# Optimization experiments

Hardware: AMD Instinct MI355X
Metric: run time of the kernel (lower is better)

The kernel has to match this reference:

```python
import jax, jax.numpy as jnp
import numpy as np

WS, OWS, NH = 16, 24, 2          # window size, overlap window size (=int(16*0.5)+16), num heads
PAD = (OWS - WS) // 2            # unfold padding = 4


def conv2d(x, w, b):
    kh, kw = w.shape[2], w.shape[3]
    out = jax.lax.conv_general_dilated(x, w, (1, 1), [(kh // 2, kh // 2), (kw // 2, kw // 2)],
                                       dimension_numbers=('NCHW', 'OIHW', 'NCHW'))
    return out + b[None, :, None, None]


def layer_norm(x, g, b, eps=1e-5):
    m = x.mean(-1, keepdims=True)
    v = ((x - m) ** 2).mean(-1, keepdims=True)
    return (x - m) * jax.lax.rsqrt(v + eps) * g + b


def stem(depth, cw1, cb1, cw2, cb2, cw3, cb3, cw4, cb4, in_g, in_b):
    # BasicConv(1->8,k3,relu) -> (8->16,k1,relu) -> (16->16,k3,relu) -> (16->32,k1) -> InstanceNorm2d(32,affine)
    y = jax.nn.relu(conv2d(depth, cw1, cb1))
    y = jax.nn.relu(conv2d(y, cw2, cb2))
    y = jax.nn.relu(conv2d(y, cw3, cb3))
    y = conv2d(y, cw4, cb4)
    m = y.mean((2, 3), keepdims=True)
    v = ((y - m) ** 2).mean((2, 3), keepdims=True)
    return (y - m) * jax.lax.rsqrt(v + 1e-5) * in_g[None, :, None, None] + in_b[None, :, None, None]


def ocab(xq, ykv, rpi, n1g, n1b, wq, bq, wkv, bkv, rpb, wp, bp, n2g, n2b, mw1, mb1, mw2, mb2):
    # Overlapping cross-attention block (HAT-style OCAB, cross variant: q from xq, kv from ykv).
    b, c, h, w = xq.shape
    x = xq.transpose(0, 2, 3, 1)   # b h w c
    y = ykv.transpose(0, 2, 3, 1)
    shortcut = x
    q = layer_norm(x, n1g, n1b) @ wq + bq          # b h w c
    kv = layer_norm(y, n1g, n1b) @ wkv + bkv       # b h w 2c
    nhw, nww = h // WS, w // WS
    # non-overlapping query windows: (b*nw, WS*WS, c)
    qw = q.reshape(b, nhw, WS, nww, WS, c).transpose(0, 1, 3, 2, 4, 5).reshape(b * nhw * nww, WS * WS, c)
    # overlapping kv windows via unfold (patch channel order = (channel, kh, kw), same as torch unfold)
    patches = jax.lax.conv_general_dilated_patches(kv.transpose(0, 3, 1, 2), (OWS, OWS), (WS, WS),
                                                   [(PAD, PAD), (PAD, PAD)])  # b, 2c*OWS*OWS, nhw, nww
    patches = patches.reshape(b, 2, c, OWS * OWS, nhw * nww).transpose(1, 0, 4, 3, 2).reshape(2, b * nhw * nww, OWS * OWS, c)
    k, v = patches[0], patches[1]
    d = c // NH
    qh = qw.reshape(-1, WS * WS, NH, d).transpose(0, 2, 1, 3) * (d ** -0.5)
    kh = k.reshape(-1, OWS * OWS, NH, d).transpose(0, 2, 1, 3)
    vh = v.reshape(-1, OWS * OWS, NH, d).transpose(0, 2, 1, 3)
    attn = jnp.einsum('whqd,whkd->whqk', qh, kh)
    attn = attn + rpb[rpi].transpose(2, 0, 1)[None]  # rel-pos bias -> [1, NH, WS*WS, OWS*OWS]
    attn = jax.nn.softmax(attn, axis=-1)
    out = jnp.einsum('whqk,whkd->whqd', attn, vh).transpose(0, 2, 1, 3).reshape(-1, WS * WS, c)
    # window reverse
    out = out.reshape(b, nhw, nww, WS, WS, c).transpose(0, 1, 3, 2, 4, 5).reshape(b, h, w, c)
    out = out @ wp + bp + shortcut
    out = out + (jax.nn.gelu(layer_norm(out, n2g, n2b) @ mw1 + mb1) @ mw2 + mb2)  # mlp_ratio=2
    return out.transpose(0, 3, 1, 2)


def setup_inputs():
    key = jax.random.key(0)
    ks = jax.random.split(key, 16)
    B, C, H, W = 1, 32, 256, 256
    s = 0.05
    return dict(
        x=jax.random.normal(ks[0], (B, C, H, W), jnp.float32),
        depth=jax.random.normal(ks[1], (B, 1, H, W), jnp.float32),
        rpi=jax.random.randint(ks[2], (WS * WS, OWS * OWS), 0, (WS + OWS - 1) ** 2),
        cw1=jax.random.normal(ks[3], (8, 1, 3, 3)) * s, cb1=jnp.zeros(8),
        cw2=jax.random.normal(ks[4], (16, 8, 1, 1)) * s, cb2=jnp.zeros(16),
        cw3=jax.random.normal(ks[5], (16, 16, 3, 3)) * s, cb3=jnp.zeros(16),
        cw4=jax.random.normal(ks[6], (32, 16, 1, 1)) * s, cb4=jnp.zeros(32),
        in_g=jnp.ones(32), in_b=jnp.zeros(32),
        n1g=jnp.ones(C), n1b=jnp.zeros(C),
        wq=jax.random.normal(ks[7], (C, C)) * s, bq=jnp.zeros(C),
        wkv=jax.random.normal(ks[8], (C, 2 * C)) * s, bkv=jnp.zeros(2 * C),
        rpb=jax.random.normal(ks[9], ((WS + OWS - 1) ** 2, NH)) * 0.02,
        wp=jax.random.normal(ks[10], (C, C)) * s, bp=jnp.zeros(C),
        n2g=jnp.ones(C), n2b=jnp.zeros(C),
        mw1=jax.random.normal(ks[11], (C, 2 * C)) * s, mb1=jnp.zeros(2 * C),
        mw2=jax.random.normal(ks[12], (2 * C, C)) * s, mb2=jnp.zeros(C),
    )


def reference(x, depth, rpi, cw1, cb1, cw2, cb2, cw3, cb3, cw4, cb4, in_g, in_b,
              n1g, n1b, wq, bq, wkv, bkv, rpb, wp, bp, n2g, n2b, mw1, mb1, mw2, mb2):
    f = stem(depth, cw1, cb1, cw2, cb2, cw3, cb3, cw4, cb4, in_g, in_b)
    a = (n1g, n1b, wq, bq, wkv, bkv, rpb, wp, bp, n2g, n2b, mw1, mb1, mw2, mb2)
    out1 = ocab(x, f, rpi, *a)   # shared OCAB weights, called twice with swapped roles
    out2 = ocab(f, x, rpi, *a)
    return out1 + out2 + x
```

## Files before the change

### kernel.cpp

```cpp
#include <hip/hip_runtime.h>
#include <hip/hip_bf16.h>

#define HW 65536
#define KPAD 584

typedef __attribute__((ext_vector_type(8))) short bf8;
typedef __attribute__((ext_vector_type(4))) float f4;

__device__ __forceinline__ unsigned short f2b(float x) {
  unsigned int u = __float_as_uint(x);
  unsigned int r = (u + 0x7fff + ((u >> 16) & 1)) >> 16;
  return (unsigned short)r;
}
__device__ __forceinline__ unsigned int pk2(float lo, float hi) {
  return (__float_as_uint(hi) & 0xffff0000u) | (__float_as_uint(lo) >> 16);
}
__device__ __forceinline__ float ex2(float x) { return __builtin_amdgcn_exp2f(x); }

__device__ __forceinline__ void stem_front_body(
    int bx, int t, const float* __restrict__ depth,
    const float* __restrict__ cw1, const float* __restrict__ cb1,
    const float* __restrict__ cw2, const float* __restrict__ cb2,
    float* __restrict__ t2) {
  int p = bx * 256 + t;
  int y = p >> 8, x = p & 255;
  float in9[9];
#pragma unroll
  for (int ky = 0; ky < 3; ky++)
#pragma unroll
    for (int kx = 0; kx < 3; kx++) {
      int yy = y + ky - 1, xx = x + kx - 1;
      bool ok = ((unsigned)yy < 256u) && ((unsigned)xx < 256u);
      in9[ky*3+kx] = ok ? depth[yy*256+xx] : 0.f;
    }
  float t1[8];
#pragma unroll
  for (int o = 0; o < 8; o++) {
    float s = cb1[o];
#pragma unroll
    for (int i = 0; i < 9; i++) s += in9[i] * cw1[o*9+i];
    t1[o] = fmaxf(s, 0.f);
  }
#pragma unroll
  for (int o = 0; o < 16; o++) {
    float s = cb2[o];
#pragma unroll
    for (int ci = 0; ci < 8; ci++) s += t1[ci] * cw2[o*8+ci];
    t2[o*HW + p] = fmaxf(s, 0.f);
  }
}

__device__ __forceinline__ void bias_body(
    int bx, int t, const int* __restrict__ rpi,
    const float* __restrict__ rpb, float* __restrict__ biasT) {
  int idx = bx*256 + t;
  int hd = idx / 147456;
  int rem = idx - hd*147456;
  int qt = rem / 9216;
  int r2 = rem - qt*9216;
  int kb = r2 >> 6;
  int q16 = (r2 >> 2) & 15;
  int r = r2 & 3;
  int key = kb*4 + r;
  int qq = qt*16 + q16;
  biasT[idx] = (rpb[rpi[qq*576 + key]*2 + hd] - 8.0f) * 1.44269504f;
}

__device__ __forceinline__ void lnmm16_body(
    int role, int bx, int t,
    float* ws, float* gs, float* bs, float* b2s, float* as, float* bbs,
    const float* __restrict__ x, const float* __restrict__ t4,
    const float* __restrict__ part,
    const float* __restrict__ ig, const float* __restrict__ ib,
    const float* __restrict__ n1g, const float* __restrict__ n1b,
    const float* __restrict__ wq, const float* __restrict__ bq,
    const float* __restrict__ wkv, const float* __restrict__ bkv,
    float* q1, float* kv1, float* q2, float* kv2) {
  const float *src, *wm, *bo; float* dst;
  int wstride, wcol; bool ain;
  if (role < 6) { src = x;  ain = false; } else { src = t4; ain = true; }
  switch (role) {
    default:
    case 0:  wm=wq;  wstride=32; wcol=0;  bo=bq;  dst=q1;               break;
    case 1:  wm=wq;  wstride=32; wcol=16; bo=bq;  dst=q1+16*HW;         break;
    case 2: case 3: case 4: case 5:
             wm=wkv; wstride=64; wcol=16*(role-2); bo=bkv; dst=kv2+16*(role-2)*HW; break;
    case 6:  wm=wq;  wstride=32; wcol=0;  bo=bq;  dst=q2;               break;
    case 7:  wm=wq;  wstride=32; wcol=16; bo=bq;  dst=q2+16*HW;         break;
    case 8: case 9: case 10: case 11:
             wm=wkv; wstride=64; wcol=16*(role-8); bo=bkv; dst=kv1+16*(role-8)*HW; break;
  }
  for (int i = t; i < 512; i += 256) ws[i] = wm[(i>>4)*wstride + wcol + (i&15)];
  if (t < 16) b2s[t] = bo[wcol + t];
  if (t < 32) {
    gs[t] = n1g[t]; bs[t] = n1b[t];
    if (ain) {
      float s = 0.f, ss = 0.f;
#pragma unroll
      for (int k = 0; k < 16; k++) { s += part[t*16+k]; ss += part[512 + t*16+k]; }
      float m = s * (1.f/65536.f);
      float var = ss * (1.f/65536.f) - m*m;
      float a = rsqrtf(var + 1e-5f) * ig[t];
      as[t] = a; bbs[t] = ib[t] - m*a;
    }
  }
  __syncthreads();
  int p = bx*256 + t;
  float v[32]; float s = 0.f;
  if (ain) {
#pragma unroll
    for (int c = 0; c < 32; c++) { v[c] = src[c*HW+p]*as[c] + bbs[c]; s += v[c]; }
  } else {
#pragma unroll
    for (int c = 0; c < 32; c++) { v[c] = src[c*HW+p]; s += v[c]; }
  }
  float m = s * 0.03125f;
  float ss = 0.f;
#pragma unroll
  for (int c = 0; c < 32; c++) { float d = v[c]-m; ss += d*d; }
  float rs = rsqrtf(ss*0.03125f + 1e-5f);
  float acc[16];
#pragma unroll
  for (int j = 0; j < 16; j++) acc[j] = b2s[j];
#pragma unroll
  for (int c = 0; c < 32; c++) {
    float ln = (v[c]-m)*rs*gs[c] + bs[c];
    const float4* w4 = (const float4*)&ws[c*16];
#pragma unroll
    for (int j4 = 0; j4 < 4; j4++) {
      float4 w = w4[j4];
      acc[j4*4+0] += ln*w.x; acc[j4*4+1] += ln*w.y;
      acc[j4*4+2] += ln*w.z; acc[j4*4+3] += ln*w.w;
    }
  }
#pragma unroll
  for (int j = 0; j < 16; j++) dst[j*HW+p] = acc[j];
}

__global__ __launch_bounds__(256) void k_misc(
    const float* __restrict__ depth,
    const float* __restrict__ cw1, const float* __restrict__ cb1,
    const float* __restrict__ cw2, const float* __restrict__ cb2,
    float* __restrict__ t2,
    const int* __restrict__ rpi, const float* __restrict__ rpb, float* __restrict__ biasT,
    const float* __restrict__ x, const float* __restrict__ t4, const float* __restrict__ part,
    const float* __restrict__ ig, const float* __restrict__ ib,
    const float* __restrict__ n1g, const float* __restrict__ n1b,
    const float* __restrict__ wq, const float* __restrict__ bq,
    const float* __restrict__ wkv, const float* __restrict__ bkv,
    float* q1, float* kv1, float* q2, float* kv2) {
  __shared__ __align__(16) float ws[512];
  __shared__ float gs[32], bs[32], b2s[16], as[32], bbs[32];
  int id = blockIdx.x, t = threadIdx.x;
  if (id < 256) { stem_front_body(id, t, depth, cw1, cb1, cw2, cb2, t2); return; }
  if (id < 1408) { bias_body(id - 256, t, rpi, rpb, biasT); return; }
  int r = id - 1408;
  lnmm16_body(r >> 8, r & 255, t, ws, gs, bs, b2s, as, bbs,
              x, t4, part, ig, ib, n1g, n1b, wq, bq, wkv, bkv, q1, kv1, q2, kv2);
}

__global__ __launch_bounds__(256) void k_lnmmB(
    const float* __restrict__ x, const float* __restrict__ t4, const float* __restrict__ part,
    const float* __restrict__ ig, const float* __restrict__ ib,
    const float* __restrict__ n1g, const float* __restrict__ n1b,
    const float* __restrict__ wq, const float* __restrict__ bq,
    const float* __restrict__ wkv, const float* __restrict__ bkv,
    float* q1, float* kv1, float* q2, float* kv2, int ybase) {
  __shared__ __align__(16) float ws[512];
  __shared__ float gs[32], bs[32], b2s[16], as[32], bbs[32];
  lnmm16_body(ybase + blockIdx.y, blockIdx.x, threadIdx.x, ws, gs, bs, b2s, as, bbs,
              x, t4, part, ig, ib, n1g, n1b, wq, bq, wkv, bkv, q1, kv1, q2, kv2);
}

__global__ __launch_bounds__(256) void k_conv3(
    const float* __restrict__ t2, const float* __restrict__ cw3,
    const float* __restrict__ cb3, float* __restrict__ t3) {
  int t = threadIdx.x;
  int p = blockIdx.x*256 + t;
  int og = blockIdx.y;
  int y = p >> 8, x = p & 255;
  float acc[4];
#pragma unroll
  for (int o = 0; o < 4; o++) acc[o] = cb3[og*4+o];
#pragma unroll 1
  for (int tap = 0; tap < 9; tap++) {
    int ky = tap/3 - 1, kx = tap - (tap/3)*3 - 1;
    int yy = y+ky, xx = x+kx;
    bool ok = ((unsigned)yy < 256u) && ((unsigned)xx < 256u);
    int pp = yy*256+xx;
#pragma unroll
    for (int ci = 0; ci < 16; ci++) {
      float v = ok ? t2[ci*HW+pp] : 0.f;
#pragma unroll
      for (int o = 0; o < 4; o++)
        acc[o] += v * cw3[(og*4+o)*144 + ci*9 + tap];
    }
  }
#pragma unroll
  for (int o = 0; o < 4; o++) t3[(og*4+o)*HW+p] = fmaxf(acc[o], 0.f);
}

__global__ __launch_bounds__(256) void k_conv4(
    const float* __restrict__ t3, const float* __restrict__ cw4,
    const float* __restrict__ cb4, float* __restrict__ t4) {
  int t = threadIdx.x;
  int p = blockIdx.x*256 + t;
  int og = blockIdx.y;
  float v[16];
#pragma unroll
  for (int ci = 0; ci < 16; ci++) v[ci] = t3[ci*HW+p];
#pragma unroll
  for (int o = 0; o < 8; o++) {
    int oo = og*8 + o;
    float s = cb4[oo];
#pragma unroll
    for (int ci = 0; ci < 16; ci++) s += v[ci]*cw4[oo*16+ci];
    t4[oo*HW+p] = s;
  }
}

__global__ __launch_bounds__(256) void k_instats1(const float* __restrict__ t4,
                                                  float* __restrict__ part) {
  int c = blockIdx.x >> 4, seg = blockIdx.x & 15;
  const float4* src = (const float4*)(t4 + c*HW + seg*4096);
  float s = 0.f, ss = 0.f;
  for (int i = threadIdx.x; i < 1024; i += 256) {
    float4 v = src[i];
    s  += v.x + v.y + v.z + v.w;
    ss += v.x*v.x + v.y*v.y + v.z*v.z + v.w*v.w;
  }
#pragma unroll
  for (int off = 32; off > 0; off >>= 1) {
    s  += __shfl_down(s, off, 64);
    ss += __shfl_down(ss, off, 64);
  }
  __shared__ float sh[8];
  int wid = threadIdx.x >> 6;
  if ((threadIdx.x & 63) == 0) { sh[wid] = s; sh[4+wid] = ss; }
  __syncthreads();
  if (threadIdx.x == 0) {
    part[blockIdx.x]       = sh[0]+sh[1]+sh[2]+sh[3];
    part[512 + blockIdx.x] = sh[4]+sh[5]+sh[6]+sh[7];
  }
}

__global__ __launch_bounds__(256, 4) void k_attn(
    const float* __restrict__ qA, const float* __restrict__ kvA, float* __restrict__ aoA,
    const float* __restrict__ qB, const float* __restrict__ kvB, float* __restrict__ aoB,
    const float* __restrict__ biasT) {
  __shared__ __align__(16) unsigned short Ks[576*16];
  __shared__ __align__(16) unsigned short Vt[16*KPAD];

  const float* q  = blockIdx.y ? qB  : qA;
  const float* kv = blockIdx.y ? kvB : kvA;
  float* ao       = blockIdx.y ? aoB : aoA;

  int id = blockIdx.x;
  int lin = ((id & 7) << 6) | (id >> 3);
  int wi = lin >> 1, hd = lin & 1;
  int wy = wi >> 4, wx = wi & 15;
  int t = threadIdx.x;
  int by = wy*16 - 4, bx = wx*16 - 4;
  int kbase = hd*16*HW, vbase = (32 + hd*16)*HW;

  int wave = t >> 6, lane = t & 63;
  int quad = lane >> 4, l16 = lane & 15;
  const bf8 zero8 = {0,0,0,0,0,0,0,0};

  bf8 qf[4];
#pragma unroll
  for (int qi = 0; qi < 4; qi++) {
    int qt = wave*4 + qi;
    if (quad < 2) {
      int prow = (wy*16 + qt)*256 + wx*16 + l16;
      unsigned short qtmp[8];
#pragma unroll
      for (int j = 0; j < 8; j++)
        qtmp[j] = f2b(q[(hd*16 + quad*8 + j)*HW + prow] * 0.360673503f);
      qf[qi] = *(const bf8*)qtmp;
    } else {
      qf[qi] = zero8;
    }
  }

  for (int e = t; e < 576; e += 256) {
    int dy = e / 24, dx = e - dy*24;
    int yy = by + dy, xx = bx + dx;
    bool ok = ((unsigned)yy < 256u) && ((unsigned)xx < 256u);
    int pp = yy*256 + xx;
    int off = e & 31;
    int ppos = ((off & 12) << 1) + ((off >> 4) << 2) + (off & 3);
    int vcol = (e & ~31) + ppos;
    unsigned short tk[16];
#pragma unroll
    for (int i = 0; i < 16; i++) {
      float kvl = ok ? kv[kbase + i*HW + pp] : 0.f;
      float vvl = ok ? kv[vbase + i*HW + pp] : 0.f;
      tk[i] = f2b(kvl);
      Vt[i*KPAD + vcol] = f2b(vvl);
    }
    *(uint4*)&Ks[e*16]     = *(uint4*)&tk[0];
    *(uint4*)&Ks[e*16 + 8] = *(uint4*)&tk[8];
  }
  __syncthreads();

  f4 oacc[4];
  float lr[4];
  const float* bb[4];
#pragma unroll
  for (int qi = 0; qi < 4; qi++) {
    int qt = wave*4 + qi;
    oacc[qi] = (f4){0.f,0.f,0.f,0.f};
    lr[qi] = 0.f;
    bb[qi] = biasT + (hd*16 + qt)*9216 + quad*64 + l16*4;
  }

#pragma unroll 2
  for (int kt2 = 0; kt2 < 18; kt2++) {
    int k0 = kt2 * 32;
    bf8 kf0 = zero8, kf1 = zero8;
    if (quad < 2) {
      kf0 = *(const bf8*)&Ks[(k0 + l16)*16 + quad*8];
      kf1 = *(const bf8*)&Ks[(k0 + 16 + l16)*16 + quad*8];
    }
    bf8 vf = *(const bf8*)&Vt[l16*KPAD + k0 + quad*8];
#pragma unroll
    for (int qi = 0; qi < 4; qi++) {
      f4 b0 = *(const f4*)&bb[qi][k0*16];
      f4 b1 = *(const f4*)&bb[qi][(k0+16)*16];
      f4 s0 = __builtin_amdgcn_mfma_f32_16x16x32_bf16(kf0, qf[qi], b0, 0, 0, 0);
      f4 s1 = __builtin_amdgcn_mfma_f32_16x16x32_bf16(kf1, qf[qi], b1, 0, 0, 0);
      float p0[4], p1[4];
#pragma unroll
      for (int r = 0; r < 4; r++) {
        p0[r] = ex2(s0[r]);
        p1[r] = ex2(s1[r]);
        lr[qi] += p0[r] + p1[r];
      }
      union { unsigned int u[4]; bf8 v; } P;
      P.u[0] = pk2(p0[0], p0[1]); P.u[1] = pk2(p0[2], p0[3]);
      P.u[2] = pk2(p1[0], p1[1]); P.u[3] = pk2(p1[2], p1[3]);
      oacc[qi] = __builtin_amdgcn_mfma_f32_16x16x32_bf16(P.v, vf, oacc[qi], 0, 0, 0);
    }
  }
#pragma unroll
  for (int qi = 0; qi < 4; qi++) {
    lr[qi] += __shfl_xor(lr[qi], 16, 64);
    lr[qi] += __shfl_xor(lr[qi], 32, 64);
  }
#pragma unroll
  for (int qi = 0; qi < 4; qi++) {
    int qt = wave*4 + qi;
#pragma unroll
    for (int r = 0; r < 4; r++) {
      float lv = __shfl(lr[qi], quad*4 + r, 64);
      int qw = qt*16 + quad*4 + r;
      ao[(hd*16 + l16)*HW + (wy*16 + (qw >> 4))*256 + wx*16 + (qw & 15)] = oacc[qi][r] / lv;
    }
  }
}

__global__ __launch_bounds__(256) void k_projmlp(
    const float* __restrict__ ao1, const float* __restrict__ ao2,
    const float* __restrict__ x, const float* __restrict__ t4,
    const float* __restrict__ part,
    const float* __restrict__ ig, const float* __restrict__ ib,
    const float* __restrict__ wp, const float* __restrict__ bp,
    const float* __restrict__ n2g, const float* __restrict__ n2b,
    const float* __restrict__ mw1, const float* __restrict__ mb1,
    const float* __restrict__ mw2, const float* __restrict__ mb2,
    float* __restrict__ o1, float* __restrict__ o2, int obase) {
  int oc = blockIdx.y + obase;
  const float* ao = oc ? ao2 : ao1;
  float* dst      = oc ? o2  : o1;
  __shared__ __align__(16) float wps[1024];
  __shared__ __align__(16) float w1s[2048];
  __shared__ __align__(16) float w2s[2048];
  __shared__ float bps[32], b1s[64], b2s[32], gs[32], bs[32], as[32], bbs[32];
  int t = threadIdx.x;
  for (int i = t; i < 1024; i += 256) wps[i] = wp[i];
  for (int i = t; i < 2048; i += 256) { w1s[i] = mw1[i]; w2s[i] = mw2[i]; }
  if (t < 64) b1s[t] = mb1[t];
  if (t < 32) {
    bps[t] = bp[t]; b2s[t] = mb2[t]; gs[t] = n2g[t]; bs[t] = n2b[t];
    float s = 0.f, ss = 0.f;
#pragma unroll
    for (int k = 0; k < 16; k++) { s += part[t*16+k]; ss += part[512 + t*16+k]; }
    float m = s * (1.f/65536.f);
    float var = ss * (1.f/65536.f) - m*m;
    float a = rsqrtf(var + 1e-5f) * ig[t];
    as[t] = a; bbs[t] = ib[t] - m*a;
  }
  __syncthreads();
  int p = blockIdx.x*256 + t;
  float acc[32];
#pragma unroll
  for (int j = 0; j < 32; j++) acc[j] = bps[j];
#pragma unroll
  for (int c = 0; c < 32; c++) {
    float vc = ao[c*HW+p];
    const float4* w4 = (const float4*)&wps[c*32];
#pragma unroll
    for (int j4 = 0; j4 < 8; j4++) {
      float4 w = w4[j4];
      acc[j4*4+0] += vc*w.x; acc[j4*4+1] += vc*w.y;
      acc[j4*4+2] += vc*w.z; acc[j4*4+3] += vc*w.w;
    }
  }
  if (oc == 0) {
#pragma unroll
    for (int j = 0; j < 32; j++) acc[j] += x[j*HW+p];
  } else {
#pragma unroll
    for (int j = 0; j < 32; j++) acc[j] += t4[j*HW+p]*as[j] + bbs[j];
  }
  float s = 0.f;
#pragma unroll
  for (int j = 0; j < 32; j++) s += acc[j];
  float m = s * 0.03125f;
  float ss = 0.f;
#pragma unroll
  for (int j = 0; j < 32; j++) { float d = acc[j]-m; ss += d*d; }
  float rs = rsqrtf(ss*0.03125f + 1e-5f);
  float r[32];
#pragma unroll
  for (int j = 0; j < 32; j++) r[j] = b2s[j];
#pragma unroll 1
  for (int half = 0; half < 2; half++) {
    float h[32];
#pragma unroll
    for (int k = 0; k < 32; k++) h[k] = b1s[half*32 + k];
#pragma unroll
    for (int c = 0; c < 32; c++) {
      float ln = (acc[c] - m) * rs * gs[c] + bs[c];
      const float4* w4 = (const float4*)&w1s[c*64 + half*32];
#pragma unroll
      for (int k4 = 0; k4 < 8; k4++) {
        float4 w = w4[k4];
        h[k4*4+0] += ln*w.x; h[k4*4+1] += ln*w.y; h[k4*4+2] += ln*w.z; h[k4*4+3] += ln*w.w;
      }
    }
#pragma unroll
    for (int k = 0; k < 32; k++) {
      float xx = h[k];
      float u = 0.7978845608f * (xx + 0.044715f*xx*xx*xx);
      float th = 1.f - 2.f/(1.f + __expf(2.f*u));
      h[k] = 0.5f * xx * (1.f + th);
    }
#pragma unroll
    for (int k = 0; k < 32; k++) {
      float hk = h[k];
      const float4* w4 = (const float4*)&w2s[(half*32 + k)*32];
#pragma unroll
      for (int j4 = 0; j4 < 8; j4++) {
        float4 w = w4[j4];
        r[j4*4+0] += hk*w.x; r[j4*4+1] += hk*w.y; r[j4*4+2] += hk*w.z; r[j4*4+3] += hk*w.w;
      }
    }
  }
#pragma unroll
  for (int j = 0; j < 32; j++) dst[j*HW + p] = acc[j] + r[j];
}

__global__ __launch_bounds__(256) void k_final(
    const float* o1, const float* __restrict__ o2,
    const float* __restrict__ x, float* out) {
  int i = blockIdx.x*256 + threadIdx.x;
  float4 a = ((const float4*)o1)[i];
  float4 b = ((const float4*)o2)[i];
  float4 c = ((const float4*)x)[i];
  float4 r;
  r.x = a.x + b.x + c.x; r.y = a.y + b.y + c.y;
  r.z = a.z + b.z + c.z; r.w = a.w + b.w + c.w;
  ((float4*)out)[i] = r;
}

extern "C" void kernel_launch(void* const* d_in, const int* in_sizes, int n_in,
                              void* d_out, int out_size, void* d_ws, size_t ws_size,
                              hipStream_t stream) {
  const float* x    = (const float*)d_in[0];
  const float* depth= (const float*)d_in[1];
  const int*   rpi  = (const int*)d_in[2];
  const float* cw1  = (const float*)d_in[3],  *cb1 = (const float*)d_in[4];
  const float* cw2  = (const float*)d_in[5],  *cb2 = (const float*)d_in[6];
  const float* cw3  = (const float*)d_in[7],  *cb3 = (const float*)d_in[8];
  const float* cw4  = (const float*)d_in[9],  *cb4 = (const float*)d_in[10];
  const float* in_g = (const float*)d_in[11], *in_b = (const float*)d_in[12];
  const float* n1g  = (const float*)d_in[13], *n1b = (const float*)d_in[14];
  const float* wq   = (const float*)d_in[15], *bq  = (const float*)d_in[16];
  const float* wkv  = (const float*)d_in[17], *bkv = (const float*)d_in[18];
  const float* rpb  = (const float*)d_in[19];
  const float* wp   = (const float*)d_in[20], *bp  = (const float*)d_in[21];
  const float* n2g  = (const float*)d_in[22], *n2b = (const float*)d_in[23];
  const float* mw1  = (const float*)d_in[24], *mb1 = (const float*)d_in[25];
  const float* mw2  = (const float*)d_in[26], *mb2 = (const float*)d_in[27];

  float* W   = (float*)d_ws;
  float* o1  = (float*)d_out;

  bool big = ws_size >= (size_t)85100000;

  if (big) {
    float* t4    = W;
    float* q1    = W + 2097152;
    float* q2    = W + 4194304;
    float* kv1   = W + 6291456;
    float* kv2   = W + 10485760;
    float* ao1   = W + 14680064;
    float* ao2   = W + 16777216;
    float* o2    = W + 18874368;
    float* biasT = W + 20971520;
    float* part  = W + 21266432;
    float* t2 = ao1, *t3 = q2;

    k_misc   <<<2944, 256, 0, stream>>>(depth, cw1, cb1, cw2, cb2, t2,
                                        rpi, rpb, biasT,
                                        x, t4, part, in_g, in_b, n1g, n1b,
                                        wq, bq, wkv, bkv, q1, kv1, q2, kv2);
    k_conv3  <<<dim3(256,4), 256, 0, stream>>>(t2, cw3, cb3, t3);
    k_conv4  <<<dim3(256,4), 256, 0, stream>>>(t3, cw4, cb4, t4);
    k_instats1<<<512, 256, 0, stream>>>(t4, part);
    k_lnmmB  <<<dim3(256,6), 256, 0, stream>>>(x, t4, part, in_g, in_b, n1g, n1b,
                                               wq, bq, wkv, bkv, q1, kv1, q2, kv2, 6);
    k_attn   <<<dim3(512,2), 256, 0, stream>>>(q1, kv1, ao1, q2, kv2, ao2, biasT);
    k_projmlp<<<dim3(256,2), 256, 0, stream>>>(ao1, ao2, x, t4, part, in_g, in_b,
                                               wp, bp, n2g, n2b, mw1, mb1, mw2, mb2,
                                               o1, o2, 0);
    k_final  <<<2048, 256, 0, stream>>>(o1, o2, x, o1);
  } else {
    float* t4    = W;
    float* q1    = W + 2097152;
    float* kv1   = W + 4194304;
    float* ao1   = W + 8388608;
    float* o2    = W + 10485760;
    float* biasT = W + 12582912;
    float* part  = W + 12877824;
    float* t2 = ao1, *t3 = o2;

    k_misc   <<<1920, 256, 0, stream>>>(depth, cw1, cb1, cw2, cb2, t2,
                                        rpi, rpb, biasT,
                                        x, t4, part, in_g, in_b, n1g, n1b,
                                        wq, bq, wkv, bkv, q1, kv1, q1, kv1);
    k_conv3  <<<dim3(256,4), 256, 0, stream>>>(t2, cw3, cb3, t3);
    k_conv4  <<<dim3(256,4), 256, 0, stream>>>(t3, cw4, cb4, t4);
    k_instats1<<<512, 256, 0, stream>>>(t4, part);
    k_lnmmB  <<<dim3(256,4), 256, 0, stream>>>(x, t4, part, in_g, in_b, n1g, n1b,
                                               wq, bq, wkv, bkv, q1, kv1, q1, kv1, 8);
    k_attn   <<<dim3(512,1), 256, 0, stream>>>(q1, kv1, ao1, q1, kv1, ao1, biasT);
    k_projmlp<<<dim3(256,1), 256, 0, stream>>>(ao1, ao1, x, t4, part, in_g, in_b,
                                               wp, bp, n2g, n2b, mw1, mb1, mw2, mb2,
                                               o1, o2, 0);
    k_lnmmB  <<<dim3(256,6), 256, 0, stream>>>(x, t4, part, in_g, in_b, n1g, n1b,
                                               wq, bq, wkv, bkv, q1, kv1, q1, kv1, 2);
    k_attn   <<<dim3(512,1), 256, 0, stream>>>(q1, kv1, ao1, q1, kv1, ao1, biasT);
    k_projmlp<<<dim3(256,1), 256, 0, stream>>>(ao1, ao1, x, t4, part, in_g, in_b,
                                               wp, bp, n2g, n2b, mw1, mb1, mw2, mb2,
                                               o1, o2, 1);
    k_final  <<<2048, 256, 0, stream>>>(o1, o2, x, o1);
  }
}
```

Before: 258.9 us.

## Fuse conv3, conv4 and instance-norm statistics into one kernel with atomics

Merges the 3x3 conv, the 1x1 conv and the instance-norm statistics pass into a single kernel. Each block computes all 16 conv3 channels in registers, then half of the conv4 outputs, and reduces per-channel sum and sum of squares with wave shuffles plus a global atomicAdd into a 64-float buffer that is zeroed by a memset. This removes the t3 round trip through memory and the separate stats read of t4, and the consumers read the final sums directly instead of adding 16 partials. In exchange conv3 is computed twice (once per half) and float atomics make the summation order nondeterministic.

```diff
diff --git a/kernel.cpp b/kernel.cpp
--- a/kernel.cpp
+++ b/kernel.cpp
@@ -95,11 +95,8 @@
   if (t < 32) {
     gs[t] = n1g[t]; bs[t] = n1b[t];
     if (ain) {
-      float s = 0.f, ss = 0.f;
-#pragma unroll
-      for (int k = 0; k < 16; k++) { s += part[t*16+k]; ss += part[512 + t*16+k]; }
-      float m = s * (1.f/65536.f);
-      float var = ss * (1.f/65536.f) - m*m;
+      float m = part[t] * (1.f/65536.f);
+      float var = part[32+t] * (1.f/65536.f) - m*m;
       float a = rsqrtf(var + 1e-5f) * ig[t];
       as[t] = a; bbs[t] = ib[t] - m*a;
     }
@@ -172,16 +169,19 @@
               x, t4, part, ig, ib, n1g, n1b, wq, bq, wkv, bkv, q1, kv1, q2, kv2);
 }
 
-__global__ __launch_bounds__(256) void k_conv3(
-    const float* __restrict__ t2, const float* __restrict__ cw3,
-    const float* __restrict__ cb3, float* __restrict__ t3) {
+__global__ __launch_bounds__(256) void k_conv34(
+    const float* __restrict__ t2,
+    const float* __restrict__ cw3, const float* __restrict__ cb3,
+    const float* __restrict__ cw4, const float* __restrict__ cb4,
+    float* __restrict__ t4, float* __restrict__ part) {
+  __shared__ float sh[128];
   int t = threadIdx.x;
-  int p = blockIdx.x*256 + t;
-  int og = blockIdx.y;
+  int bx = blockIdx.x, half = blockIdx.y;
+  int p = bx*256 + t;
   int y = p >> 8, x = p & 255;
-  float acc[4];
-#pragma unroll
-  for (int o = 0; o < 4; o++) acc[o] = cb3[og*4+o];
+  float a3[16];
+#pragma unroll
+  for (int o = 0; o < 16; o++) a3[o] = cb3[o];
 #pragma unroll 1
   for (int tap = 0; tap < 9; tap++) {
     int ky = tap/3 - 1, kx = tap - (tap/3)*3 - 1;
@@ -192,55 +192,34 @@
     for (int ci = 0; ci < 16; ci++) {
       float v = ok ? t2[ci*HW+pp] : 0.f;
 #pragma unroll
-      for (int o = 0; o < 4; o++)
-        acc[o] += v * cw3[(og*4+o)*144 + ci*9 + tap];
-    }
-  }
-#pragma unroll
-  for (int o = 0; o < 4; o++) t3[(og*4+o)*HW+p] = fmaxf(acc[o], 0.f);
-}
-
-__global__ __launch_bounds__(256) void k_conv4(
-    const float* __restrict__ t3, const float* __restrict__ cw4,
-    const float* __restrict__ cb4, float* __restrict__ t4) {
-  int t = threadIdx.x;
-  int p = blockIdx.x*256 + t;
-  int og = blockIdx.y;
-  float v[16];
-#pragma unroll
-  for (int ci = 0; ci < 16; ci++) v[ci] = t3[ci*HW+p];
-#pragma unroll
-  for (int o = 0; o < 8; o++) {
-    int oo = og*8 + o;
+      for (int o = 0; o < 16; o++)
+        a3[o] += v * cw3[o*144 + ci*9 + tap];
+    }
+  }
+#pragma unroll
+  for (int o = 0; o < 16; o++) a3[o] = fmaxf(a3[o], 0.f);
+  int wave = t >> 6;
+#pragma unroll 1
+  for (int o = 0; o < 16; o++) {
+    int oo = half*16 + o;
     float s = cb4[oo];
 #pragma unroll
-    for (int ci = 0; ci < 16; ci++) s += v[ci]*cw4[oo*16+ci];
+    for (int ci = 0; ci < 16; ci++) s += a3[ci]*cw4[oo*16+ci];
     t4[oo*HW+p] = s;
-  }
-}
-
-__global__ __launch_bounds__(256) void k_instats1(const float* __restrict__ t4,
-                                                  float* __restrict__ part) {
-  int c = blockIdx.x >> 4, seg = blockIdx.x & 15;
-  const float4* src = (const float4*)(t4 + c*HW + seg*4096);
-  float s = 0.f, ss = 0.f;
-  for (int i = threadIdx.x; i < 1024; i += 256) {
-    float4 v = src[i];
-    s  += v.x + v.y + v.z + v.w;
-    ss += v.x*v.x + v.y*v.y + v.z*v.z + v.w*v.w;
-  }
-#pragma unroll
-  for (int off = 32; off > 0; off >>= 1) {
-    s  += __shfl_down(s, off, 64);
-    ss += __shfl_down(ss, off, 64);
-  }
-  __shared__ float sh[8];
-  int wid = threadIdx.x >> 6;
-  if ((threadIdx.x & 63) == 0) { sh[wid] = s; sh[4+wid] = ss; }
+    float sum = s, ssq = s*s;
+#pragma unroll
+    for (int off = 32; off > 0; off >>= 1) {
+      sum += __shfl_down(sum, off, 64);
+      ssq += __shfl_down(ssq, off, 64);
+    }
+    if ((t & 63) == 0) { sh[o*4 + wave] = sum; sh[64 + o*4 + wave] = ssq; }
+  }
   __syncthreads();
-  if (threadIdx.x == 0) {
-    part[blockIdx.x]       = sh[0]+sh[1]+sh[2]+sh[3];
-    part[512 + blockIdx.x] = sh[4]+sh[5]+sh[6]+sh[7];
+  if (t < 32) {
+    int o = t & 15, kind = t >> 4;
+    float v = sh[kind*64 + o*4+0] + sh[kind*64 + o*4+1]
+            + sh[kind*64 + o*4+2] + sh[kind*64 + o*4+3];
+    atomicAdd(&part[kind*32 + half*16 + o], v);
   }
 }
 
@@ -383,11 +362,8 @@
   if (t < 64) b1s[t] = mb1[t];
   if (t < 32) {
     bps[t] = bp[t]; b2s[t] = mb2[t]; gs[t] = n2g[t]; bs[t] = n2b[t];
-    float s = 0.f, ss = 0.f;
-#pragma unroll
-    for (int k = 0; k < 16; k++) { s += part[t*16+k]; ss += part[512 + t*16+k]; }
-    float m = s * (1.f/65536.f);
-    float var = ss * (1.f/65536.f) - m*m;
+    float m = part[t] * (1.f/65536.f);
+    float var = part[32+t] * (1.f/65536.f) - m*m;
     float a = rsqrtf(var + 1e-5f) * ig[t];
     as[t] = a; bbs[t] = ib[t] - m*a;
   }
@@ -511,15 +487,14 @@
     float* o2    = W + 18874368;
     float* biasT = W + 20971520;
     float* part  = W + 21266432;
-    float* t2 = ao1, *t3 = q2;
-
+    float* t2 = ao1;
+
+    hipMemsetAsync(part, 0, 64*sizeof(float), stream);
     k_misc   <<<2944, 256, 0, stream>>>(depth, cw1, cb1, cw2, cb2, t2,
                                         rpi, rpb, biasT,
                                         x, t4, part, in_g, in_b, n1g, n1b,
                                         wq, bq, wkv, bkv, q1, kv1, q2, kv2);
-    k_conv3  <<<dim3(256,4), 256, 0, stream>>>(t2, cw3, cb3, t3);
-    k_conv4  <<<dim3(256,4), 256, 0, stream>>>(t3, cw4, cb4, t4);
-    k_instats1<<<512, 256, 0, stream>>>(t4, part);
+    k_conv34 <<<dim3(256,2), 256, 0, stream>>>(t2, cw3, cb3, cw4, cb4, t4, part);
     k_lnmmB  <<<dim3(256,6), 256, 0, stream>>>(x, t4, part, in_g, in_b, n1g, n1b,
                                                wq, bq, wkv, bkv, q1, kv1, q2, kv2, 6);
     k_attn   <<<dim3(512,2), 256, 0, stream>>>(q1, kv1, ao1, q2, kv2, ao2, biasT);
@@ -535,15 +510,14 @@
     float* o2    = W + 10485760;
     float* biasT = W + 12582912;
     float* part  = W + 12877824;
-    float* t2 = ao1, *t3 = o2;
-
+    float* t2 = ao1;
+
+    hipMemsetAsync(part, 0, 64*sizeof(float), stream);
     k_misc   <<<1920, 256, 0, stream>>>(depth, cw1, cb1, cw2, cb2, t2,
                                         rpi, rpb, biasT,
                                         x, t4, part, in_g, in_b, n1g, n1b,
                                         wq, bq, wkv, bkv, q1, kv1, q1, kv1);
-    k_conv3  <<<dim3(256,4), 256, 0, stream>>>(t2, cw3, cb3, t3);
-    k_conv4  <<<dim3(256,4), 256, 0, stream>>>(t3, cw4, cb4, t4);
-    k_instats1<<<512, 256, 0, stream>>>(t4, part);
+    k_conv34 <<<dim3(256,2), 256, 0, stream>>>(t2, cw3, cb3, cw4, cb4, t4, part);
     k_lnmmB  <<<dim3(256,4), 256, 0, stream>>>(x, t4, part, in_g, in_b, n1g, n1b,
                                                wq, bq, wkv, bkv, q1, kv1, q1, kv1, 8);
     k_attn   <<<dim3(512,1), 256, 0, stream>>>(q1, kv1, ao1, q1, kv1, ao1, biasT);
```

New measurement: 307.4 us. +18.8%, slower.
